# Optimization experiments

Measured on AMD Instinct MI355X. Metric: run time of the kernel, lower is better.

Reference implementation:

```python
import jax, jax.numpy as jnp
import numpy as np
import math

B, S, D = 4, 2048, 1024
H = 16
DH = D // H
NEG = -1e20


def setup_inputs() -> dict:
    key = jax.random.key(0)
    ks = jax.random.split(key, 8)
    Q_batch = jax.random.normal(ks[0], (B, S, D), dtype=jnp.float32)
    K_batch = jax.random.normal(ks[1], (B, S, D), dtype=jnp.float32)
    V_batch = jax.random.normal(ks[2], (B, S, D), dtype=jnp.float32)
    valid_lens = jax.random.randint(ks[3], (B,), 0, S).astype(jnp.int64)
    # LazyLinear weights, stored as (in, out) so projection is x @ W
    sc = 1.0 / math.sqrt(D)
    Wq = jax.random.normal(ks[4], (D, D), dtype=jnp.float32) * sc
    Wk = jax.random.normal(ks[5], (D, D), dtype=jnp.float32) * sc
    Wv = jax.random.normal(ks[6], (D, D), dtype=jnp.float32) * sc
    Wo = jax.random.normal(ks[7], (D, D), dtype=jnp.float32) * sc
    return {"Q_batch": Q_batch, "K_batch": K_batch, "V_batch": V_batch,
            "valid_lens": valid_lens, "Wq": Wq, "Wk": Wk, "Wv": Wv, "Wo": Wo}


def reference(Q_batch, K_batch, V_batch, valid_lens, Wq, Wk, Wv, Wo):
    b, nq, _ = Q_batch.shape
    nk = K_batch.shape[1]
    # project and split heads (feature dim split head-major, matching transpose_qkv)
    q = (Q_batch @ Wq).reshape(b, nq, H, DH).transpose(0, 2, 1, 3)  # (b,h,nq,dh)
    k = (K_batch @ Wk).reshape(b, nk, H, DH).transpose(0, 2, 1, 3)  # (b,h,nk,dh)
    v = (V_batch @ Wv).reshape(b, nk, H, DH).transpose(0, 2, 1, 3)  # (b,h,nk,dh)
    scores = jnp.einsum('bhqd,bhkd->bhqk', q, k) / math.sqrt(DH)
    # mask keys at position >= valid_lens[b] (shared across heads and queries)
    key_pos = jnp.arange(nk)
    mask = key_pos[None, None, None, :] < valid_lens[:, None, None, None]
    scores = jnp.where(mask, scores, NEG)
    w = jax.nn.softmax(scores, axis=-1)  # dropout rate 0 -> identity
    o = jnp.einsum('bhqk,bhkd->bhqd', w, v)           # (b,h,nq,dh)
    o = o.transpose(0, 2, 1, 3).reshape(b, nq, H * DH)  # concat heads
    return o @ Wo
```

## Files before the change

kernel.cpp:

```cpp
#include <hip/hip_runtime.h>
#include <stdint.h>

typedef unsigned short u16;
using bf16x8 = __attribute__((ext_vector_type(8))) __bf16;
using f32x4  = __attribute__((ext_vector_type(4))) float;
using u16x8  = __attribute__((ext_vector_type(8))) unsigned short;
using u16x4  = __attribute__((ext_vector_type(4))) unsigned short;

#define NH   16
#define DHD  64
#define SEQ  2048
#define DD   1024

__device__ inline u16 bfbits(float f) {
    __bf16 h = (__bf16)f;
    return __builtin_bit_cast(u16, h);
}

__device__ inline void gld16(const u16* g, u16* l) {
    __builtin_amdgcn_global_load_lds(
        (const __attribute__((address_space(1))) void*)g,
        (__attribute__((address_space(3))) void*)l,
        16, 0, 0);
}

__global__ __launch_bounds__(256) void transpose4(
    const float* __restrict__ s0, const float* __restrict__ s1,
    const float* __restrict__ s2, const float* __restrict__ s3,
    u16* __restrict__ d0, u16* __restrict__ d1,
    u16* __restrict__ d2, u16* __restrict__ d3)
{
    const float* src = s0; u16* dst = d0;
    if (blockIdx.z == 1) { src = s1; dst = d1; }
    else if (blockIdx.z == 2) { src = s2; dst = d2; }
    else if (blockIdx.z == 3) { src = s3; dst = d3; }

    __shared__ u16 tile[32][33];
    int tx = threadIdx.x, ty = threadIdx.y;
    int x = blockIdx.x * 32 + tx;
    int y0 = blockIdx.y * 32 + ty;
#pragma unroll
    for (int i = 0; i < 32; i += 8)
        tile[ty + i][tx] = bfbits(src[(size_t)(y0 + i) * DD + x]);
    __syncthreads();
    int x2 = blockIdx.y * 32 + tx;
    int y2 = blockIdx.x * 32 + ty;
#pragma unroll
    for (int i = 0; i < 32; i += 8)
        dst[(size_t)(y2 + i) * DD + x2] = tile[tx][ty + i];
}

__global__ __launch_bounds__(256) void cvt3(
    const float* __restrict__ s0, const float* __restrict__ s1,
    const float* __restrict__ s2,
    u16* __restrict__ d0, u16* __restrict__ d1, u16* __restrict__ d2)
{
    const float* src = s0; u16* dst = d0;
    if (blockIdx.z == 1) { src = s1; dst = d1; }
    else if (blockIdx.z == 2) { src = s2; dst = d2; }
    size_t i = ((size_t)blockIdx.x * 256 + threadIdx.x) * 8;
    f32x4 a = *(const f32x4*)&src[i];
    f32x4 b = *(const f32x4*)&src[i + 4];
    u16x8 o;
#pragma unroll
    for (int j = 0; j < 4; ++j) { o[j] = bfbits(a[j]); o[j + 4] = bfbits(b[j]); }
    *(u16x8*)&dst[i] = o;
}

__global__ __launch_bounds__(256) void cvt1(
    const float* __restrict__ src, u16* __restrict__ dst)
{
    size_t i = ((size_t)blockIdx.x * 256 + threadIdx.x) * 8;
    f32x4 a = *(const f32x4*)&src[i];
    f32x4 b = *(const f32x4*)&src[i + 4];
    u16x8 o;
#pragma unroll
    for (int j = 0; j < 4; ++j) { o[j] = bfbits(a[j]); o[j + 4] = bfbits(b[j]); }
    *(u16x8*)&dst[i] = o;
}

template<int MODE>
__global__ __launch_bounds__(256) void gemm_bt16(
    const u16* __restrict__ A0, const u16* __restrict__ A1, const u16* __restrict__ A2,
    const u16* __restrict__ B0, const u16* __restrict__ B1, const u16* __restrict__ B2,
    void* __restrict__ C0, void* __restrict__ C1, void* __restrict__ C2)
{
    const int K = 1024;
    const u16* A = A0; const u16* Bt = B0; void* C = C0;
    if (MODE == 3) {
        if (blockIdx.z == 1) { A = A1; Bt = B1; C = C1; }
        else if (blockIdx.z == 2) { A = A2; Bt = B2; C = C2; }
    }

    __shared__ __align__(16) u16 As[2][128 * 32];
    __shared__ __align__(16) u16 Bs[2][128 * 32];

    const int t = threadIdx.x;
    const int wave = t >> 6, lane = t & 63;
    const int l15 = lane & 15, q4 = lane >> 4;
    const int wm = (wave >> 1) * 64, wn = (wave & 1) * 64;

    const int gx = gridDim.x;
    const int nwg = gx * gridDim.y;
    int flat = blockIdx.y * gx + blockIdx.x;
    flat = (flat & 7) * (nwg >> 3) + (flat >> 3);
    const int m0 = (flat / gx) * 128, n0 = (flat % gx) * 128;

    const int ar = t >> 2;
    const int ac = (t & 3) * 8;

    const u16* gA = &A [(size_t)(m0 + ar) * K + ac];
    const u16* gB = &Bt[(size_t)(n0 + ar) * K + ac];
    u16* lA0 = &As[0][t * 8];
    u16* lA1 = &As[1][t * 8];
    u16* lB0 = &Bs[0][t * 8];
    u16* lB1 = &Bs[1][t * 8];

    f32x4 acc[4][4] = {};

    for (int k0 = 0; k0 < K; k0 += 64) {
        __syncthreads();
        gld16(gA + k0,                   lA0);
        gld16(gA + (size_t)64 * K + k0,  lA0 + 64 * 32);
        gld16(gA + k0 + 32,              lA1);
        gld16(gA + (size_t)64 * K + k0 + 32, lA1 + 64 * 32);
        gld16(gB + k0,                   lB0);
        gld16(gB + (size_t)64 * K + k0,  lB0 + 64 * 32);
        gld16(gB + k0 + 32,              lB1);
        gld16(gB + (size_t)64 * K + k0 + 32, lB1 + 64 * 32);
        __syncthreads();

#pragma unroll
        for (int hf = 0; hf < 2; ++hf) {
            bf16x8 af[4], bfr[4];
#pragma unroll
            for (int i = 0; i < 4; ++i) {
                af[i]  = *(const bf16x8*)&As[hf][(wm + i * 16 + l15) * 32 + q4 * 8];
                bfr[i] = *(const bf16x8*)&Bs[hf][(wn + i * 16 + l15) * 32 + q4 * 8];
            }
#pragma unroll
            for (int i = 0; i < 4; ++i)
#pragma unroll
                for (int j = 0; j < 4; ++j)
                    acc[i][j] = __builtin_amdgcn_mfma_f32_16x16x32_bf16(af[i], bfr[j], acc[i][j], 0, 0, 0);
        }
    }

    const bool vt_store = (MODE == 2) || (MODE == 3 && blockIdx.z == 2);

#pragma unroll
    for (int i = 0; i < 4; ++i) {
        int row_l = wm + i * 16 + q4 * 4;
#pragma unroll
        for (int j = 0; j < 4; ++j) {
            int col = n0 + wn + j * 16 + l15;
            if (MODE == 1) {
#pragma unroll
                for (int r = 0; r < 4; ++r) {
                    int row = m0 + row_l + r;
                    ((float*)C)[(size_t)row * DD + col] = acc[i][j][r];
                }
            } else if (vt_store) {
                int row = m0 + row_l;
                int b = row >> 11, s = row & (SEQ - 1);
                int h = col >> 6, dh = col & (DHD - 1);
                u16x4 pk;
#pragma unroll
                for (int r = 0; r < 4; ++r) pk[r] = bfbits(acc[i][j][r]);
                *(u16x4*)&((u16*)C)[(((size_t)(b * NH + h) * DHD + dh) << 11) | s] = pk;
            } else {
#pragma unroll
                for (int r = 0; r < 4; ++r) {
                    int row = m0 + row_l + r;
                    int b = row >> 11, s = row & (SEQ - 1);
                    int h = col >> 6, dh = col & (DHD - 1);
                    ((u16*)C)[(((size_t)(b * NH + h) * SEQ + s) << 6) | dh] = bfbits(acc[i][j][r]);
                }
            }
        }
    }
}

__global__ __launch_bounds__(256, 4) void attn(
    const u16* __restrict__ q_ws, const u16* __restrict__ k_ws,
    const u16* __restrict__ vT_ws, const int* __restrict__ valid_lens,
    u16* __restrict__ o_ws)
{
    const int bh = blockIdx.y;
    const int b = bh >> 4, h = bh & 15;
    const int qt = blockIdx.x;
    const int valid = valid_lens[b];
    const bool valid0 = (valid == 0);
    const int valid_eff = valid0 ? SEQ : valid;
    const int kt_n = (valid_eff + 63) >> 6;
    const float c2 = valid0 ? 0.f : 0.18033688011112042f;
    const float M2 = 17.312340490667562f;

    __shared__ __align__(16) u16 Kbuf[2][64 * 64];
    __shared__ __align__(16) u16 Vbuf[64 * 64];
    __shared__ __align__(16) u16 Ps[4][32][64];

    const int t = threadIdx.x;
    const int wave = t >> 6, lane = t & 63;
    const int l15 = lane & 15, q4 = lane >> 4;

    const size_t base  = (size_t)bh * SEQ * DHD;
    const size_t vbase = (size_t)bh * DHD * SEQ;

    const int q0 = qt * 128 + wave * 32;

    const int sr0 = wave * 16 + (lane >> 3);
    const int cg  = ((lane & 7) ^ (sr0 & 7)) * 8;
    const u16* gK = &k_ws [base  + (size_t)sr0 * DHD + cg];
    const u16* gV = &vT_ws[vbase + (size_t)sr0 * SEQ + cg];
    const int ldst = sr0 * 64 + (lane & 7) * 8;

    u16x8 ou;
#pragma unroll
    for (int j = 0; j < 8; ++j) ou[j] = 0x3F80;
    const bf16x8 ones = __builtin_bit_cast(bf16x8, ou);

    bf16x8 qf[2][2];
#pragma unroll
    for (int mi = 0; mi < 2; ++mi)
#pragma unroll
        for (int c = 0; c < 2; ++c)
            qf[mi][c] = *(const bf16x8*)&q_ws[base + (size_t)(q0 + mi * 16 + l15) * DHD + c * 32 + q4 * 8];

    f32x4 o4[2][4] = {};
    f32x4 l_acc[2] = {};

    const int swz  = (l15 & 7) * 8;

    gld16(gK,       &Kbuf[0][ldst]);
    gld16(gK + 512, &Kbuf[0][ldst + 512]);

    int cur = 0;
    for (int kt = 0; kt < kt_n; ++kt) {
        __syncthreads();
        {
            const u16* vv = gV + (size_t)kt * 64;
            gld16(vv,                   &Vbuf[ldst]);
            gld16(vv + (size_t)8 * SEQ, &Vbuf[ldst + 512]);
        }
        const bool pre = (kt + 1 < kt_n);
        if (pre) {
            const u16* kk = gK + (size_t)(kt + 1) * 64 * DHD;
            int bf = cur ^ 1;
            gld16(kk,       &Kbuf[bf][ldst]);
            gld16(kk + 512, &Kbuf[bf][ldst + 512]);
        }

        const u16* KK = Kbuf[cur];

        f32x4 s4[2][4] = {};
#pragma unroll
        for (int c = 0; c < 2; ++c)
#pragma unroll
            for (int ni = 0; ni < 4; ++ni) {
                bf16x8 kf = *(const bf16x8*)&KK[(ni * 16 + l15) * 64 + ((c * 32 + q4 * 8) ^ swz)];
#pragma unroll
                for (int mi = 0; mi < 2; ++mi)
                    s4[mi][ni] = __builtin_amdgcn_mfma_f32_16x16x32_bf16(kf, qf[mi][c], s4[mi][ni], 0, 0, 0);
            }

        const bool tile_full = valid0 || (kt * 64 + 64 <= valid_eff);
        if (tile_full) {
#pragma unroll
            for (int mi = 0; mi < 2; ++mi) {
                int qrow = mi * 16 + l15;
                int psw  = (l15 & 7) * 8;
#pragma unroll
                for (int ni = 0; ni < 4; ++ni) {
                    u16x4 pk;
#pragma unroll
                    for (int r = 0; r < 4; ++r) {
                        float p = __builtin_amdgcn_exp2f(__builtin_fmaf(s4[mi][ni][r], c2, -M2));
                        pk[r] = bfbits(p);
                    }
                    *(u16x4*)&Ps[wave][qrow][(ni * 16 + q4 * 4) ^ psw] = pk;
                }
            }
        } else {
#pragma unroll
            for (int mi = 0; mi < 2; ++mi) {
                int qrow = mi * 16 + l15;
                int psw  = (l15 & 7) * 8;
#pragma unroll
                for (int ni = 0; ni < 4; ++ni) {
                    u16x4 pk;
#pragma unroll
                    for (int r = 0; r < 4; ++r) {
                        bool ok = (kt * 64 + ni * 16 + q4 * 4 + r) < valid_eff;
                        float arg = ok ? __builtin_fmaf(s4[mi][ni][r], c2, -M2) : -1e30f;
                        pk[r] = bfbits(__builtin_amdgcn_exp2f(arg));
                    }
                    *(u16x4*)&Ps[wave][qrow][(ni * 16 + q4 * 4) ^ psw] = pk;
                }
            }
        }

        if (pre) asm volatile("s_waitcnt vmcnt(2)\n\ts_barrier" ::: "memory");
        else     asm volatile("s_waitcnt vmcnt(0)\n\ts_barrier" ::: "memory");

#pragma unroll
        for (int c = 0; c < 2; ++c) {
            bf16x8 pf[2];
#pragma unroll
            for (int mi = 0; mi < 2; ++mi) {
                pf[mi] = *(const bf16x8*)&Ps[wave][mi * 16 + l15][(c * 32 + q4 * 8) ^ ((l15 & 7) * 8)];
                l_acc[mi] = __builtin_amdgcn_mfma_f32_16x16x32_bf16(pf[mi], ones, l_acc[mi], 0, 0, 0);
            }
#pragma unroll
            for (int dt = 0; dt < 4; ++dt) {
                bf16x8 vf = *(const bf16x8*)&Vbuf[(dt * 16 + l15) * 64 + ((c * 32 + q4 * 8) ^ swz)];
#pragma unroll
                for (int mi = 0; mi < 2; ++mi)
                    o4[mi][dt] = __builtin_amdgcn_mfma_f32_16x16x32_bf16(pf[mi], vf, o4[mi][dt], 0, 0, 0);
            }
        }
        cur ^= 1;
    }

#pragma unroll
    for (int mi = 0; mi < 2; ++mi) {
        float inv[4];
#pragma unroll
        for (int r = 0; r < 4; ++r) inv[r] = 1.0f / l_acc[mi][r];
        int qrow = q0 + mi * 16 + q4 * 4;
#pragma unroll
        for (int dt = 0; dt < 4; ++dt) {
            int dh = dt * 16 + l15;
#pragma unroll
            for (int r = 0; r < 4; ++r) {
                float v = o4[mi][dt][r] * inv[r];
                o_ws[((size_t)(b * SEQ + qrow + r) << 10) | (h * DHD + dh)] = bfbits(v);
            }
        }
    }
}

extern "C" void kernel_launch(void* const* d_in, const int* in_sizes, int n_in,
                              void* d_out, int out_size, void* d_ws, size_t ws_size,
                              hipStream_t stream)
{
    (void)in_sizes; (void)n_in; (void)out_size;
    const float* Q  = (const float*)d_in[0];
    const float* Kb = (const float*)d_in[1];
    const float* V  = (const float*)d_in[2];
    const int*   vl = (const int*)d_in[3];
    const float* Wq = (const float*)d_in[4];
    const float* Wk = (const float*)d_in[5];
    const float* Wv = (const float*)d_in[6];
    const float* Wo = (const float*)d_in[7];
    float* out = (float*)d_out;

    char* ws = (char*)d_ws;
    u16* WqT   = (u16*)(ws + (size_t)0);
    u16* WkT   = (u16*)(ws + ((size_t)2 << 20));
    u16* WvT   = (u16*)(ws + ((size_t)4 << 20));
    u16* WoT   = (u16*)(ws + ((size_t)6 << 20));
    u16* q_ws  = (u16*)(ws + ((size_t)8 << 20));
    u16* k_ws  = (u16*)(ws + ((size_t)24 << 20));
    u16* vT_ws = (u16*)(ws + ((size_t)40 << 20));
    u16* o_ws  = (u16*)(ws + ((size_t)56 << 20));
    u16* Qbf   = (u16*)(ws + ((size_t)72 << 20));
    u16* Kbf   = (u16*)(ws + ((size_t)88 << 20));
    u16* Vbf   = (u16*)(ws + ((size_t)104 << 20));

    transpose4<<<dim3(32, 32, 4), dim3(32, 8), 0, stream>>>(
        Wq, Wk, Wv, Wo, WqT, WkT, WvT, WoT);

    const bool fused = ws_size >= ((size_t)120 << 20);
    if (fused) {
        cvt3<<<dim3(4096, 1, 3), 256, 0, stream>>>(Q, Kb, V, Qbf, Kbf, Vbf);
        gemm_bt16<3><<<dim3(8, 64, 3), 256, 0, stream>>>(
            Qbf, Kbf, Vbf, WqT, WkT, WvT, q_ws, k_ws, vT_ws);
    } else {
        cvt1<<<4096, 256, 0, stream>>>(Q, o_ws);
        gemm_bt16<0><<<dim3(8, 64), 256, 0, stream>>>(
            o_ws, nullptr, nullptr, WqT, nullptr, nullptr, q_ws, nullptr, nullptr);
        cvt1<<<4096, 256, 0, stream>>>(Kb, o_ws);
        gemm_bt16<0><<<dim3(8, 64), 256, 0, stream>>>(
            o_ws, nullptr, nullptr, WkT, nullptr, nullptr, k_ws, nullptr, nullptr);
        cvt1<<<4096, 256, 0, stream>>>(V, o_ws);
        gemm_bt16<2><<<dim3(8, 64), 256, 0, stream>>>(
            o_ws, nullptr, nullptr, WvT, nullptr, nullptr, vT_ws, nullptr, nullptr);
    }

    attn<<<dim3(16, 64), 256, 0, stream>>>(q_ws, k_ws, vT_ws, vl, o_ws);

    gemm_bt16<1><<<dim3(8, 64), 256, 0, stream>>>(
        o_ws, nullptr, nullptr, WoT, nullptr, nullptr, out, nullptr, nullptr);
}
```

Baseline: 303.2 us.

## Fuse fp32-to-bf16 input conversion into the QKV projection GEMM

Removes the separate cvt3 pass and its bf16 staging buffers. A new gemm_qkv kernel loads fp32 activations into registers, converts them to bf16 and writes them into LDS, while the weights still stream in through global_load_lds. The next tile's fp32 A data is prefetched into registers to overlap with compute. This drops one launch and a full write and read of the bf16 copies, but doubles the global bytes read per A tile and adds register pressure and conversion work inside the GEMM loop.

```diff
diff --git a/kernel.cpp b/kernel.cpp
--- a/kernel.cpp
+++ b/kernel.cpp
@@ -50,14 +50,9 @@
         dst[(size_t)(y2 + i) * DD + x2] = tile[tx][ty + i];
 }
 
-__global__ __launch_bounds__(256) void cvt3(
-    const float* __restrict__ s0, const float* __restrict__ s1,
-    const float* __restrict__ s2,
-    u16* __restrict__ d0, u16* __restrict__ d1, u16* __restrict__ d2)
-{
-    const float* src = s0; u16* dst = d0;
-    if (blockIdx.z == 1) { src = s1; dst = d1; }
-    else if (blockIdx.z == 2) { src = s2; dst = d2; }
+__global__ __launch_bounds__(256) void cvt1(
+    const float* __restrict__ src, u16* __restrict__ dst)
+{
     size_t i = ((size_t)blockIdx.x * 256 + threadIdx.x) * 8;
     f32x4 a = *(const f32x4*)&src[i];
     f32x4 b = *(const f32x4*)&src[i + 4];
@@ -67,30 +62,14 @@
     *(u16x8*)&dst[i] = o;
 }
 
-__global__ __launch_bounds__(256) void cvt1(
-    const float* __restrict__ src, u16* __restrict__ dst)
-{
-    size_t i = ((size_t)blockIdx.x * 256 + threadIdx.x) * 8;
-    f32x4 a = *(const f32x4*)&src[i];
-    f32x4 b = *(const f32x4*)&src[i + 4];
-    u16x8 o;
-#pragma unroll
-    for (int j = 0; j < 4; ++j) { o[j] = bfbits(a[j]); o[j + 4] = bfbits(b[j]); }
-    *(u16x8*)&dst[i] = o;
-}
-
 template<int MODE>
 __global__ __launch_bounds__(256) void gemm_bt16(
-    const u16* __restrict__ A0, const u16* __restrict__ A1, const u16* __restrict__ A2,
-    const u16* __restrict__ B0, const u16* __restrict__ B1, const u16* __restrict__ B2,
-    void* __restrict__ C0, void* __restrict__ C1, void* __restrict__ C2)
+    const u16* __restrict__ A0,
+    const u16* __restrict__ B0,
+    void* __restrict__ C0)
 {
     const int K = 1024;
     const u16* A = A0; const u16* Bt = B0; void* C = C0;
-    if (MODE == 3) {
-        if (blockIdx.z == 1) { A = A1; Bt = B1; C = C1; }
-        else if (blockIdx.z == 2) { A = A2; Bt = B2; C = C2; }
-    }
 
     __shared__ __align__(16) u16 As[2][128 * 32];
     __shared__ __align__(16) u16 Bs[2][128 * 32];
@@ -146,8 +125,6 @@
         }
     }
 
-    const bool vt_store = (MODE == 2) || (MODE == 3 && blockIdx.z == 2);
-
 #pragma unroll
     for (int i = 0; i < 4; ++i) {
         int row_l = wm + i * 16 + q4 * 4;
@@ -160,7 +137,7 @@
                     int row = m0 + row_l + r;
                     ((float*)C)[(size_t)row * DD + col] = acc[i][j][r];
                 }
-            } else if (vt_store) {
+            } else if (MODE == 2) {
                 int row = m0 + row_l;
                 int b = row >> 11, s = row & (SEQ - 1);
                 int h = col >> 6, dh = col & (DHD - 1);
@@ -175,6 +152,132 @@
                     int b = row >> 11, s = row & (SEQ - 1);
                     int h = col >> 6, dh = col & (DHD - 1);
                     ((u16*)C)[(((size_t)(b * NH + h) * SEQ + s) << 6) | dh] = bfbits(acc[i][j][r]);
+                }
+            }
+        }
+    }
+}
+
+__global__ __launch_bounds__(256) void gemm_qkv(
+    const float* __restrict__ A0, const float* __restrict__ A1,
+    const float* __restrict__ A2,
+    const u16* __restrict__ B0, const u16* __restrict__ B1,
+    const u16* __restrict__ B2,
+    u16* __restrict__ C0, u16* __restrict__ C1, u16* __restrict__ C2)
+{
+    const int K = 1024;
+    const float* A = A0; const u16* Bt = B0; u16* C = C0;
+    if (blockIdx.z == 1) { A = A1; Bt = B1; C = C1; }
+    else if (blockIdx.z == 2) { A = A2; Bt = B2; C = C2; }
+
+    __shared__ __align__(16) u16 As[2][128 * 32];
+    __shared__ __align__(16) u16 Bs[2][128 * 32];
+
+    const int t = threadIdx.x;
+    const int wave = t >> 6, lane = t & 63;
+    const int l15 = lane & 15, q4 = lane >> 4;
+    const int wm = (wave >> 1) * 64, wn = (wave & 1) * 64;
+
+    const int gx = gridDim.x;
+    const int nwg = gx * gridDim.y;
+    int flat = blockIdx.y * gx + blockIdx.x;
+    flat = (flat & 7) * (nwg >> 3) + (flat >> 3);
+    const int m0 = (flat / gx) * 128, n0 = (flat % gx) * 128;
+
+    const int ar = t >> 2;
+    const int ac = (t & 3) * 8;
+
+    const float* gAf = &A [(size_t)(m0 + ar) * K + ac];
+    const u16*   gB  = &Bt[(size_t)(n0 + ar) * K + ac];
+    u16* lB0 = &Bs[0][t * 8];
+    u16* lB1 = &Bs[1][t * 8];
+
+    f32x4 areg[8];
+#pragma unroll
+    for (int p = 0; p < 4; ++p) {
+        const float* src = gAf + (p >> 1) * 32 + (size_t)(p & 1) * 64 * K;
+        areg[2 * p]     = *(const f32x4*)src;
+        areg[2 * p + 1] = *(const f32x4*)(src + 4);
+    }
+
+    f32x4 acc[4][4] = {};
+
+    for (int k0 = 0; k0 < K; k0 += 64) {
+        asm volatile("s_waitcnt lgkmcnt(0)" ::: "memory");
+        __builtin_amdgcn_s_barrier();
+        asm volatile("s_waitcnt vmcnt(0)" ::: "memory");
+        __builtin_amdgcn_sched_barrier(0);
+
+#pragma unroll
+        for (int p = 0; p < 4; ++p) {
+            u16x8 w;
+#pragma unroll
+            for (int j = 0; j < 4; ++j) {
+                w[j]     = bfbits(areg[2 * p][j]);
+                w[j + 4] = bfbits(areg[2 * p + 1][j]);
+            }
+            *(u16x8*)&As[p >> 1][t * 8 + (p & 1) * 2048] = w;
+        }
+        gld16(gB + k0,                       lB0);
+        gld16(gB + (size_t)64 * K + k0,      lB0 + 2048);
+        gld16(gB + k0 + 32,                  lB1);
+        gld16(gB + (size_t)64 * K + k0 + 32, lB1 + 2048);
+        __builtin_amdgcn_sched_barrier(0);
+
+        const bool pre = (k0 + 64 < K);
+        if (pre) {
+#pragma unroll
+            for (int p = 0; p < 4; ++p) {
+                const float* src = gAf + (k0 + 64) + (p >> 1) * 32 + (size_t)(p & 1) * 64 * K;
+                areg[2 * p]     = *(const f32x4*)src;
+                areg[2 * p + 1] = *(const f32x4*)(src + 4);
+            }
+        }
+        __builtin_amdgcn_sched_barrier(0);
+        if (pre) asm volatile("s_waitcnt vmcnt(8) lgkmcnt(0)" ::: "memory");
+        else     asm volatile("s_waitcnt vmcnt(0) lgkmcnt(0)" ::: "memory");
+        __builtin_amdgcn_sched_barrier(0);
+        __builtin_amdgcn_s_barrier();
+
+#pragma unroll
+        for (int hf = 0; hf < 2; ++hf) {
+            bf16x8 af[4], bfr[4];
+#pragma unroll
+            for (int i = 0; i < 4; ++i) {
+                af[i]  = *(const bf16x8*)&As[hf][(wm + i * 16 + l15) * 32 + q4 * 8];
+                bfr[i] = *(const bf16x8*)&Bs[hf][(wn + i * 16 + l15) * 32 + q4 * 8];
+            }
+#pragma unroll
+            for (int i = 0; i < 4; ++i)
+#pragma unroll
+                for (int j = 0; j < 4; ++j)
+                    acc[i][j] = __builtin_amdgcn_mfma_f32_16x16x32_bf16(af[i], bfr[j], acc[i][j], 0, 0, 0);
+        }
+    }
+
+    const bool vt_store = (blockIdx.z == 2);
+
+#pragma unroll
+    for (int i = 0; i < 4; ++i) {
+        int row_l = wm + i * 16 + q4 * 4;
+#pragma unroll
+        for (int j = 0; j < 4; ++j) {
+            int col = n0 + wn + j * 16 + l15;
+            if (vt_store) {
+                int row = m0 + row_l;
+                int b = row >> 11, s = row & (SEQ - 1);
+                int h = col >> 6, dh = col & (DHD - 1);
+                u16x4 pk;
+#pragma unroll
+                for (int r = 0; r < 4; ++r) pk[r] = bfbits(acc[i][j][r]);
+                *(u16x4*)&C[(((size_t)(b * NH + h) * DHD + dh) << 11) | s] = pk;
+            } else {
+#pragma unroll
+                for (int r = 0; r < 4; ++r) {
+                    int row = m0 + row_l + r;
+                    int b = row >> 11, s = row & (SEQ - 1);
+                    int h = col >> 6, dh = col & (DHD - 1);
+                    C[(((size_t)(b * NH + h) * SEQ + s) << 6) | dh] = bfbits(acc[i][j][r]);
                 }
             }
         }
@@ -364,32 +467,24 @@
     u16* k_ws  = (u16*)(ws + ((size_t)24 << 20));
     u16* vT_ws = (u16*)(ws + ((size_t)40 << 20));
     u16* o_ws  = (u16*)(ws + ((size_t)56 << 20));
-    u16* Qbf   = (u16*)(ws + ((size_t)72 << 20));
-    u16* Kbf   = (u16*)(ws + ((size_t)88 << 20));
-    u16* Vbf   = (u16*)(ws + ((size_t)104 << 20));
 
     transpose4<<<dim3(32, 32, 4), dim3(32, 8), 0, stream>>>(
         Wq, Wk, Wv, Wo, WqT, WkT, WvT, WoT);
 
     const bool fused = ws_size >= ((size_t)120 << 20);
     if (fused) {
-        cvt3<<<dim3(4096, 1, 3), 256, 0, stream>>>(Q, Kb, V, Qbf, Kbf, Vbf);
-        gemm_bt16<3><<<dim3(8, 64, 3), 256, 0, stream>>>(
-            Qbf, Kbf, Vbf, WqT, WkT, WvT, q_ws, k_ws, vT_ws);
+        gemm_qkv<<<dim3(8, 64, 3), 256, 0, stream>>>(
+            Q, Kb, V, WqT, WkT, WvT, q_ws, k_ws, vT_ws);
     } else {
         cvt1<<<4096, 256, 0, stream>>>(Q, o_ws);
-        gemm_bt16<0><<<dim3(8, 64), 256, 0, stream>>>(
-            o_ws, nullptr, nullptr, WqT, nullptr, nullptr, q_ws, nullptr, nullptr);
+        gemm_bt16<0><<<dim3(8, 64), 256, 0, stream>>>(o_ws, WqT, q_ws);
         cvt1<<<4096, 256, 0, stream>>>(Kb, o_ws);
-        gemm_bt16<0><<<dim3(8, 64), 256, 0, stream>>>(
-            o_ws, nullptr, nullptr, WkT, nullptr, nullptr, k_ws, nullptr, nullptr);
+        gemm_bt16<0><<<dim3(8, 64), 256, 0, stream>>>(o_ws, WkT, k_ws);
         cvt1<<<4096, 256, 0, stream>>>(V, o_ws);
-        gemm_bt16<2><<<dim3(8, 64), 256, 0, stream>>>(
-            o_ws, nullptr, nullptr, WvT, nullptr, nullptr, vT_ws, nullptr, nullptr);
+        gemm_bt16<2><<<dim3(8, 64), 256, 0, stream>>>(o_ws, WvT, vT_ws);
     }
 
     attn<<<dim3(16, 64), 256, 0, stream>>>(q_ws, k_ws, vT_ws, vl, o_ws);
 
-    gemm_bt16<1><<<dim3(8, 64), 256, 0, stream>>>(
-        o_ws, nullptr, nullptr, WoT, nullptr, nullptr, out, nullptr, nullptr);
-}
+    gemm_bt16<1><<<dim3(8, 64), 256, 0, stream>>>(o_ws, WoT, out);
+}
```

Measured after the change: 322.7 us. 1.06x slower.
